# Kernel tuning notes

Hardware: AMD Instinct MI355X
Metric: run time of the kernel (lower is better)

The kernel has to match this reference:

```python
import jax, jax.numpy as jnp
import numpy as np

VOCAB = 30000
EMB = 128
ENC = 128
BS = 256
DEPTH = 10            # perfect binary tree depth
N = 2 ** DEPTH - 1    # 1023 nodes per tree, heap layout: children of i are 2i+1, 2i+2


def setup_inputs() -> dict:
    key = jax.random.key(0)
    k1, k2, k3, k4 = jax.random.split(key, 4)
    tokens = jax.random.randint(k1, (BS, N), 0, VOCAB)                       # node token ids
    emb = jax.random.normal(k2, (VOCAB, EMB), jnp.float32) * 0.02            # embedding table
    W_c = jax.random.normal(k3, (ENC, EMB), jnp.float32) / np.sqrt(EMB)      # Linear weight [out,in]
    b_c = jax.random.normal(k4, (ENC,), jnp.float32) * 0.01                  # Linear bias
    return {"tokens": tokens, "emb": emb, "W_c": W_c, "b_c": b_c, "bs": BS}


def reference(tokens, emb, W_c, b_c, bs):
    # Per-node leaf contribution: c = W_c(embedding(token))  -> [bs, N, ENC]
    c = jnp.einsum('bne,oe->bno', emb[tokens], W_c) + b_c
    # Bottom-up tree sum: h[i] = c[i] + h[2i+1] + h[2i+2]
    h = c
    for l in reversed(range(DEPTH - 1)):          # fixed small loop over tree depth
        s = 2 ** l - 1
        e = 2 ** (l + 1) - 1
        left = h[:, 2 * s + 1:2 * e:2]            # children of parents [s, e)
        right = h[:, 2 * s + 2:2 * e + 1:2]
        h = h.at[:, s:e].add(left + right)
    # Max-pool over all nodes of each tree (original: max over stacked node_list)
    return jnp.max(h, axis=1)                     # [bs, ENC]
```

## Files before the change

kernel.cpp:

```cpp
#include <hip/hip_runtime.h>
#include <hip/hip_bf16.h>
#include <stdint.h>

#define VOCAB 30000
#define EMB 128
#define ENC 128
#define BS 256
#define NNODES 1023

typedef short short8 __attribute__((ext_vector_type(8)));
typedef float f32x4 __attribute__((ext_vector_type(4)));

__device__ __forceinline__ unsigned short f2bf(float x) {
    uint32_t u = __float_as_uint(x);
    uint32_t r = u + 0x7fffu + ((u >> 16) & 1u);
    return (unsigned short)(r >> 16);
}
__device__ __forceinline__ float bf2f(unsigned short h) {
    return __uint_as_float(((uint32_t)h) << 16);
}

#define WLD 136
__global__ void __launch_bounds__(256) project_k(const float* __restrict__ emb,
                                                 const float* __restrict__ W,
                                                 const float* __restrict__ bias,
                                                 unsigned short* __restrict__ P) {
    __shared__ unsigned short Wlds[ENC * WLD];

    for (int i = threadIdx.x; i < ENC * EMB; i += 256) {
        const int o = i >> 7, k = i & 127;
        Wlds[o * WLD + k] = f2bf(W[i]);
    }
    __syncthreads();

    const int wave = threadIdx.x >> 6;
    const int lane = threadIdx.x & 63;
    const int r = lane & 15;
    const int q = lane >> 4;
    const int v0 = blockIdx.x * 64 + wave * 16;

    int vr = v0 + r;
    if (vr > VOCAB - 1) vr = VOCAB - 1;

    short8 af[4];
    const float* erow = emb + (size_t)vr * EMB + q * 8;
#pragma unroll
    for (int kk = 0; kk < 4; kk++) {
        const float4 x0 = *(const float4*)(erow + kk * 32);
        const float4 x1 = *(const float4*)(erow + kk * 32 + 4);
        short8 a;
        a[0] = (short)f2bf(x0.x); a[1] = (short)f2bf(x0.y);
        a[2] = (short)f2bf(x0.z); a[3] = (short)f2bf(x0.w);
        a[4] = (short)f2bf(x1.x); a[5] = (short)f2bf(x1.y);
        a[6] = (short)f2bf(x1.z); a[7] = (short)f2bf(x1.w);
        af[kk] = a;
    }

#pragma unroll
    for (int ot = 0; ot < 8; ot++) {
        const int o0 = ot * 16;
        f32x4 acc = {0.f, 0.f, 0.f, 0.f};
        const unsigned short* wrow = Wlds + (o0 + r) * WLD + q * 8;
#pragma unroll
        for (int kk = 0; kk < 4; kk++) {
            short8 bf = *(const short8*)(wrow + kk * 32);
            acc = __builtin_amdgcn_mfma_f32_16x16x32_bf16(af[kk], bf, acc, 0, 0, 0);
        }
        const float bb = bias[o0 + r];
#pragma unroll
        for (int i = 0; i < 4; i++) {
            const int vo = v0 + q * 4 + i;
            if (vo < VOCAB) P[(size_t)vo * ENC + o0 + r] = f2bf(acc[i] + bb);
        }
    }
}

__global__ void subtree_k(const int* __restrict__ tokens, const unsigned short* __restrict__ P,
                          float* __restrict__ sums, float* __restrict__ maxes) {
    const int st = blockIdx.x;
    const int b  = blockIdx.y;
    const int ch = threadIdx.x;
    const int* tb = tokens + b * NNODES;
    const int rp1 = 32 + st;

    float m = -3.0e38f;
    float v[16];
    int base = (rp1 << 4) - 1;
#pragma unroll
    for (int i = 0; i < 16; i++) v[i] = bf2f(P[tb[base + i] * ENC + ch]);
#pragma unroll
    for (int i = 0; i < 16; i++) m = fmaxf(m, v[i]);

    float u[8];
    base = (rp1 << 3) - 1;
#pragma unroll
    for (int i = 0; i < 8; i++) {
        u[i] = bf2f(P[tb[base + i] * ENC + ch]) + v[2 * i] + v[2 * i + 1];
        m = fmaxf(m, u[i]);
    }
    float w4[4];
    base = (rp1 << 2) - 1;
#pragma unroll
    for (int i = 0; i < 4; i++) {
        w4[i] = bf2f(P[tb[base + i] * ENC + ch]) + u[2 * i] + u[2 * i + 1];
        m = fmaxf(m, w4[i]);
    }
    float w2[2];
    base = (rp1 << 1) - 1;
#pragma unroll
    for (int i = 0; i < 2; i++) {
        w2[i] = bf2f(P[tb[base + i] * ENC + ch]) + w4[2 * i] + w4[2 * i + 1];
        m = fmaxf(m, w2[i]);
    }
    const float s = bf2f(P[tb[rp1 - 1] * ENC + ch]) + w2[0] + w2[1];
    m = fmaxf(m, s);

    const int idx = (b * 32 + st) * ENC + ch;
    sums[idx] = s;
    maxes[idx] = m;
}

__global__ void topfold_k(const int* __restrict__ tokens, const unsigned short* __restrict__ P,
                          const float* __restrict__ sums, const float* __restrict__ maxes,
                          float* __restrict__ out) {
    const int b = blockIdx.x;
    const int ch = threadIdx.x;
    const int* tb = tokens + b * NNODES;

    float m = -3.0e38f;
    float v[32];
#pragma unroll
    for (int i = 0; i < 32; i++) v[i] = sums[(b * 32 + i) * ENC + ch];
#pragma unroll
    for (int i = 0; i < 32; i++) m = fmaxf(m, maxes[(b * 32 + i) * ENC + ch]);

    float u[16];
#pragma unroll
    for (int i = 0; i < 16; i++) {
        u[i] = bf2f(P[tb[15 + i] * ENC + ch]) + v[2 * i] + v[2 * i + 1];
        m = fmaxf(m, u[i]);
    }
    float w8[8];
#pragma unroll
    for (int i = 0; i < 8; i++) {
        w8[i] = bf2f(P[tb[7 + i] * ENC + ch]) + u[2 * i] + u[2 * i + 1];
        m = fmaxf(m, w8[i]);
    }
    float w4[4];
#pragma unroll
    for (int i = 0; i < 4; i++) {
        w4[i] = bf2f(P[tb[3 + i] * ENC + ch]) + w8[2 * i] + w8[2 * i + 1];
        m = fmaxf(m, w4[i]);
    }
    float w2[2];
#pragma unroll
    for (int i = 0; i < 2; i++) {
        w2[i] = bf2f(P[tb[1 + i] * ENC + ch]) + w4[2 * i] + w4[2 * i + 1];
        m = fmaxf(m, w2[i]);
    }
    const float s0 = bf2f(P[tb[0] * ENC + ch]) + w2[0] + w2[1];
    m = fmaxf(m, s0);

    out[b * ENC + ch] = m;
}

extern "C" void kernel_launch(void* const* d_in, const int* in_sizes, int n_in,
                              void* d_out, int out_size, void* d_ws, size_t ws_size,
                              hipStream_t stream) {
    const int*   tokens = (const int*)d_in[0];
    const float* emb    = (const float*)d_in[1];
    const float* W_c    = (const float*)d_in[2];
    const float* b_c    = (const float*)d_in[3];
    float* out = (float*)d_out;

    char* ws = (char*)d_ws;
    unsigned short* P     = (unsigned short*)ws;
    float*          sums  = (float*)(ws + 7680000);
    float*          maxes = sums + BS * 32 * ENC;

    project_k<<<(VOCAB + 63) / 64, 256, 0, stream>>>(emb, W_c, b_c, P);
    subtree_k<<<dim3(32, BS), 128, 0, stream>>>(tokens, P, sums, maxes);
    topfold_k<<<BS, 128, 0, stream>>>(tokens, P, sums, maxes, out);
}
```

Before: 96.01 us.

## Fuse subtree and top-fold kernels via last-block atomic counter, pack two channels per lane

Merges the subtree and top-fold kernels into one launch. The last block finishing for each tree, detected through an atomic counter plus thread fences, performs the top-level fold. Each wave now handles one subtree with 64 lanes, and each lane loads a packed pair of bf16 channels as a 32-bit word, halving the number of gather load instructions. This removes one kernel launch and its dependency gap, at the cost of a memset launch and atomic and fence overhead, and the top fold runs serialized in the last block.

```diff
diff --git a/kernel.cpp b/kernel.cpp
--- a/kernel.cpp
+++ b/kernel.cpp
@@ -75,90 +75,113 @@
     }
 }
 
-__global__ void subtree_k(const int* __restrict__ tokens, const unsigned short* __restrict__ P,
-                          float* __restrict__ sums, float* __restrict__ maxes) {
-    const int st = blockIdx.x;
-    const int b  = blockIdx.y;
+__global__ void __launch_bounds__(128) tree_k(const int* __restrict__ tokens,
+                                              const unsigned short* __restrict__ P,
+                                              float* __restrict__ sums,
+                                              float* __restrict__ maxes,
+                                              unsigned int* __restrict__ cnt,
+                                              float* __restrict__ out) {
+    const int lane = threadIdx.x & 63;
+    const int w    = threadIdx.x >> 6;
+    const int b    = blockIdx.y;
+    const int st   = blockIdx.x * 2 + w;
+    const int* tb  = tokens + b * NNODES;
+    const int rp1  = 32 + st;
+    const uint32_t* Pw = (const uint32_t*)P;
+
+    float2 m2; m2.x = -3.0e38f; m2.y = -3.0e38f;
+    float2 v[16];
+    int base = (rp1 << 4) - 1;
+#pragma unroll
+    for (int i = 0; i < 16; i++) {
+        const uint32_t p = Pw[(size_t)tb[base + i] * 64 + lane];
+        v[i].x = __uint_as_float(p << 16);
+        v[i].y = __uint_as_float(p & 0xffff0000u);
+    }
+#pragma unroll
+    for (int i = 0; i < 16; i++) { m2.x = fmaxf(m2.x, v[i].x); m2.y = fmaxf(m2.y, v[i].y); }
+
+    float2 u[8];
+    base = (rp1 << 3) - 1;
+#pragma unroll
+    for (int i = 0; i < 8; i++) {
+        const uint32_t p = Pw[(size_t)tb[base + i] * 64 + lane];
+        u[i].x = __uint_as_float(p << 16)         + v[2 * i].x + v[2 * i + 1].x;
+        u[i].y = __uint_as_float(p & 0xffff0000u) + v[2 * i].y + v[2 * i + 1].y;
+        m2.x = fmaxf(m2.x, u[i].x); m2.y = fmaxf(m2.y, u[i].y);
+    }
+    float2 w4[4];
+    base = (rp1 << 2) - 1;
+#pragma unroll
+    for (int i = 0; i < 4; i++) {
+        const uint32_t p = Pw[(size_t)tb[base + i] * 64 + lane];
+        w4[i].x = __uint_as_float(p << 16)         + u[2 * i].x + u[2 * i + 1].x;
+        w4[i].y = __uint_as_float(p & 0xffff0000u) + u[2 * i].y + u[2 * i + 1].y;
+        m2.x = fmaxf(m2.x, w4[i].x); m2.y = fmaxf(m2.y, w4[i].y);
+    }
+    float2 w2[2];
+    base = (rp1 << 1) - 1;
+#pragma unroll
+    for (int i = 0; i < 2; i++) {
+        const uint32_t p = Pw[(size_t)tb[base + i] * 64 + lane];
+        w2[i].x = __uint_as_float(p << 16)         + w4[2 * i].x + w4[2 * i + 1].x;
+        w2[i].y = __uint_as_float(p & 0xffff0000u) + w4[2 * i].y + w4[2 * i + 1].y;
+        m2.x = fmaxf(m2.x, w2[i].x); m2.y = fmaxf(m2.y, w2[i].y);
+    }
+    {
+        const uint32_t p = Pw[(size_t)tb[rp1 - 1] * 64 + lane];
+        float2 s;
+        s.x = __uint_as_float(p << 16)         + w2[0].x + w2[1].x;
+        s.y = __uint_as_float(p & 0xffff0000u) + w2[0].y + w2[1].y;
+        m2.x = fmaxf(m2.x, s.x); m2.y = fmaxf(m2.y, s.y);
+        ((float2*)(sums  + (b * 32 + st) * ENC))[lane] = s;
+        ((float2*)(maxes + (b * 32 + st) * ENC))[lane] = m2;
+    }
+
+    __shared__ int is_last;
+    __syncthreads();
+    if (threadIdx.x == 0) {
+        __threadfence();
+        const unsigned int old = atomicAdd(&cnt[b], 1u);
+        is_last = (old == 15);
+    }
+    __syncthreads();
+    if (!is_last) return;
+    __threadfence();
+
     const int ch = threadIdx.x;
-    const int* tb = tokens + b * NNODES;
-    const int rp1 = 32 + st;
-
     float m = -3.0e38f;
-    float v[16];
-    int base = (rp1 << 4) - 1;
-#pragma unroll
-    for (int i = 0; i < 16; i++) v[i] = bf2f(P[tb[base + i] * ENC + ch]);
-#pragma unroll
-    for (int i = 0; i < 16; i++) m = fmaxf(m, v[i]);
-
-    float u[8];
-    base = (rp1 << 3) - 1;
+    float vv[32];
+#pragma unroll
+    for (int i = 0; i < 32; i++) vv[i] = sums[(b * 32 + i) * ENC + ch];
+#pragma unroll
+    for (int i = 0; i < 32; i++) m = fmaxf(m, maxes[(b * 32 + i) * ENC + ch]);
+
+    float uu[16];
+#pragma unroll
+    for (int i = 0; i < 16; i++) {
+        uu[i] = bf2f(P[(size_t)tb[15 + i] * ENC + ch]) + vv[2 * i] + vv[2 * i + 1];
+        m = fmaxf(m, uu[i]);
+    }
+    float w8[8];
 #pragma unroll
     for (int i = 0; i < 8; i++) {
-        u[i] = bf2f(P[tb[base + i] * ENC + ch]) + v[2 * i] + v[2 * i + 1];
-        m = fmaxf(m, u[i]);
-    }
-    float w4[4];
-    base = (rp1 << 2) - 1;
+        w8[i] = bf2f(P[(size_t)tb[7 + i] * ENC + ch]) + uu[2 * i] + uu[2 * i + 1];
+        m = fmaxf(m, w8[i]);
+    }
+    float q4[4];
 #pragma unroll
     for (int i = 0; i < 4; i++) {
-        w4[i] = bf2f(P[tb[base + i] * ENC + ch]) + u[2 * i] + u[2 * i + 1];
-        m = fmaxf(m, w4[i]);
-    }
-    float w2[2];
-    base = (rp1 << 1) - 1;
+        q4[i] = bf2f(P[(size_t)tb[3 + i] * ENC + ch]) + w8[2 * i] + w8[2 * i + 1];
+        m = fmaxf(m, q4[i]);
+    }
+    float q2[2];
 #pragma unroll
     for (int i = 0; i < 2; i++) {
-        w2[i] = bf2f(P[tb[base + i] * ENC + ch]) + w4[2 * i] + w4[2 * i + 1];
-        m = fmaxf(m, w2[i]);
-    }
-    const float s = bf2f(P[tb[rp1 - 1] * ENC + ch]) + w2[0] + w2[1];
-    m = fmaxf(m, s);
-
-    const int idx = (b * 32 + st) * ENC + ch;
-    sums[idx] = s;
-    maxes[idx] = m;
-}
-
-__global__ void topfold_k(const int* __restrict__ tokens, const unsigned short* __restrict__ P,
-                          const float* __restrict__ sums, const float* __restrict__ maxes,
-                          float* __restrict__ out) {
-    const int b = blockIdx.x;
-    const int ch = threadIdx.x;
-    const int* tb = tokens + b * NNODES;
-
-    float m = -3.0e38f;
-    float v[32];
-#pragma unroll
-    for (int i = 0; i < 32; i++) v[i] = sums[(b * 32 + i) * ENC + ch];
-#pragma unroll
-    for (int i = 0; i < 32; i++) m = fmaxf(m, maxes[(b * 32 + i) * ENC + ch]);
-
-    float u[16];
-#pragma unroll
-    for (int i = 0; i < 16; i++) {
-        u[i] = bf2f(P[tb[15 + i] * ENC + ch]) + v[2 * i] + v[2 * i + 1];
-        m = fmaxf(m, u[i]);
-    }
-    float w8[8];
-#pragma unroll
-    for (int i = 0; i < 8; i++) {
-        w8[i] = bf2f(P[tb[7 + i] * ENC + ch]) + u[2 * i] + u[2 * i + 1];
-        m = fmaxf(m, w8[i]);
-    }
-    float w4[4];
-#pragma unroll
-    for (int i = 0; i < 4; i++) {
-        w4[i] = bf2f(P[tb[3 + i] * ENC + ch]) + w8[2 * i] + w8[2 * i + 1];
-        m = fmaxf(m, w4[i]);
-    }
-    float w2[2];
-#pragma unroll
-    for (int i = 0; i < 2; i++) {
-        w2[i] = bf2f(P[tb[1 + i] * ENC + ch]) + w4[2 * i] + w4[2 * i + 1];
-        m = fmaxf(m, w2[i]);
-    }
-    const float s0 = bf2f(P[tb[0] * ENC + ch]) + w2[0] + w2[1];
+        q2[i] = bf2f(P[(size_t)tb[1 + i] * ENC + ch]) + q4[2 * i] + q4[2 * i + 1];
+        m = fmaxf(m, q2[i]);
+    }
+    const float s0 = bf2f(P[(size_t)tb[0] * ENC + ch]) + q2[0] + q2[1];
     m = fmaxf(m, s0);
 
     out[b * ENC + ch] = m;
@@ -177,8 +200,9 @@
     unsigned short* P     = (unsigned short*)ws;
     float*          sums  = (float*)(ws + 7680000);
     float*          maxes = sums + BS * 32 * ENC;
-
+    unsigned int*   cnt   = (unsigned int*)(maxes + BS * 32 * ENC);
+
+    hipMemsetAsync(cnt, 0, BS * sizeof(unsigned int), stream);
     project_k<<<(VOCAB + 63) / 64, 256, 0, stream>>>(emb, W_c, b_c, P);
-    subtree_k<<<dim3(32, BS), 128, 0, stream>>>(tokens, P, sums, maxes);
-    topfold_k<<<BS, 128, 0, stream>>>(tokens, P, sums, maxes, out);
-}
+    tree_k<<<dim3(16, BS), 128, 0, stream>>>(tokens, P, sums, maxes, cnt, out);
+}
```

Result: slower. 251.7 us (+162.2%).
